# Optimization experiments

Hardware: AMD Instinct MI355X
Metric: run time of the kernel (lower is better)

The kernel has to match this reference:

```python
import jax, jax.numpy as jnp
import numpy as np

V, BLK, C, H, L = 50257, 1024, 1024, 16, 4
B, T = 2, 1024
D = C // H
EPS = 1e-5

def _ln(x, w):
    mu = jnp.mean(x, axis=-1, keepdims=True)
    var = jnp.mean(jnp.square(x - mu), axis=-1, keepdims=True)
    return (x - mu) * jax.lax.rsqrt(var + EPS) * w

def setup_inputs() -> dict:
    key = jax.random.key(0)
    ks = jax.random.split(key, 9)
    s = 0.02
    return {
        'idx': jax.random.randint(ks[0], (B, T), 0, V),
        'wte': jax.random.normal(ks[1], (V, C), jnp.float32) * s,
        'wpe': jax.random.normal(ks[2], (BLK, C), jnp.float32) * s,
        'ln1_w': jnp.ones((L, C), jnp.float32),
        'attn_w': jax.random.normal(ks[3], (L, 3 * C, C), jnp.float32) * s,   # torch Linear [out,in]
        'attnproj_w': jax.random.normal(ks[4], (L, C, C), jnp.float32) * (s / np.sqrt(2 * L)),
        'ln2_w': jnp.ones((L, C), jnp.float32),
        'fc_w': jax.random.normal(ks[5], (L, 4 * C, C), jnp.float32) * s,
        'mlpproj_w': jax.random.normal(ks[6], (L, C, 4 * C), jnp.float32) * (s / np.sqrt(2 * L)),
        'lnf_w': jnp.ones((C,), jnp.float32),
        'head_w': jax.random.normal(ks[7], (V, C), jnp.float32) * s,
    }

def _block(x, ln1_w, attn_w, attnproj_w, ln2_w, fc_w, mlpproj_w):
    b, t, c = x.shape
    h = _ln(x, ln1_w)
    qkv = h @ attn_w.T                                  # [B,T,3C]
    q, k, v = jnp.split(qkv, 3, axis=-1)
    q = q.reshape(b, t, H, D).transpose(0, 2, 1, 3)      # [B,H,T,D]
    k = k.reshape(b, t, H, D).transpose(0, 2, 1, 3)
    v = v.reshape(b, t, H, D).transpose(0, 2, 1, 3)
    att = jnp.einsum('bhqd,bhkd->bhqk', q, k) * (1.0 / np.sqrt(D))
    causal = jnp.tril(jnp.ones((t, t), bool))
    att = jnp.where(causal, att, jnp.float32(-jnp.inf))
    p = jax.nn.softmax(att, axis=-1)
    y = jnp.einsum('bhqk,bhkd->bhqd', p, v)
    y = y.transpose(0, 2, 1, 3).reshape(b, t, c)
    y = y @ attnproj_w.T
    x = x + y
    m = _ln(x, ln2_w)
    m = jax.nn.relu(m @ fc_w.T) @ mlpproj_w.T
    return x + m

def reference(idx, wte, wpe, ln1_w, attn_w, attnproj_w, ln2_w, fc_w, mlpproj_w, lnf_w, head_w):
    t = idx.shape[1]
    x = wte[idx] + wpe[:t]                               # [B,T,C]
    for i in range(L):
        x = _block(x, ln1_w[i], attn_w[i], attnproj_w[i], ln2_w[i], fc_w[i], mlpproj_w[i])
    x = _ln(x, lnf_w)
    return x @ head_w.T                                  # logits [B,T,V]
```

## Files before the change

### kernel.cpp

```cpp
#include <hip/hip_runtime.h>

typedef __bf16 bf16x8 __attribute__((ext_vector_type(8)));
typedef float f32x4 __attribute__((ext_vector_type(4)));
typedef unsigned short u16x8 __attribute__((ext_vector_type(8)));

#define LOG2E 1.4426950408889634f

__device__ __forceinline__ unsigned short f2bf(float f) {
  union { float f; unsigned u; } v; v.f = f;
  return (unsigned short)((v.u + 0x7fffu + ((v.u >> 16) & 1u)) >> 16);
}

__device__ __forceinline__ void gload16(const void* g, void* l) {
  __builtin_amdgcn_global_load_lds(
      (const __attribute__((address_space(1))) unsigned int*)g,
      (__attribute__((address_space(3))) unsigned int*)l, 16, 0, 0);
}

__global__ __launch_bounds__(256) void cvt_kernel(
    const float* __restrict__ s, unsigned short* __restrict__ d, int n8) {
  int i = blockIdx.x * 256 + threadIdx.x;
  int stride = gridDim.x * 256;
  for (; i < n8; i += stride) {
    float4 a = ((const float4*)s)[2 * i];
    float4 b = ((const float4*)s)[2 * i + 1];
    u16x8 o;
    o[0] = f2bf(a.x); o[1] = f2bf(a.y); o[2] = f2bf(a.z); o[3] = f2bf(a.w);
    o[4] = f2bf(b.x); o[5] = f2bf(b.y); o[6] = f2bf(b.z); o[7] = f2bf(b.w);
    ((u16x8*)d)[i] = o;
  }
}

__global__ __launch_bounds__(256) void embed_kernel(
    const int* __restrict__ idx, const float* __restrict__ wte,
    const float* __restrict__ wpe, float* __restrict__ x) {
  int row = blockIdx.x;
  int tok = idx[row];
  int t = row & 1023;
  float4 a = ((const float4*)(wte + (size_t)tok * 1024))[threadIdx.x];
  float4 p = ((const float4*)(wpe + (size_t)t * 1024))[threadIdx.x];
  a.x += p.x; a.y += p.y; a.z += p.z; a.w += p.w;
  ((float4*)(x + (size_t)row * 1024))[threadIdx.x] = a;
}

__global__ __launch_bounds__(256) void ln_kernel(
    const float* __restrict__ x, const float* __restrict__ w,
    unsigned short* __restrict__ out) {
  __shared__ float2 red[4];
  int row = blockIdx.x, tid = threadIdx.x;
  float4 v = ((const float4*)(x + (size_t)row * 1024))[tid];
  float s  = v.x + v.y + v.z + v.w;
  float s2 = v.x * v.x + v.y * v.y + v.z * v.z + v.w * v.w;
#pragma unroll
  for (int m = 32; m >= 1; m >>= 1) {
    s  += __shfl_xor(s, m, 64);
    s2 += __shfl_xor(s2, m, 64);
  }
  if ((tid & 63) == 0) red[tid >> 6] = make_float2(s, s2);
  __syncthreads();
  float S = 0.f, S2 = 0.f;
#pragma unroll
  for (int i = 0; i < 4; ++i) { S += red[i].x; S2 += red[i].y; }
  float mu = S * (1.f / 1024.f);
  float var = S2 * (1.f / 1024.f) - mu * mu;
  float rs = rsqrtf(var + 1e-5f);
  float4 wv = ((const float4*)w)[tid];
  ushort4 o;
  o.x = f2bf((v.x - mu) * rs * wv.x);
  o.y = f2bf((v.y - mu) * rs * wv.y);
  o.z = f2bf((v.z - mu) * rs * wv.z);
  o.w = f2bf((v.w - mu) * rs * wv.w);
  ((ushort4*)(out + (size_t)row * 1024))[tid] = o;
}

template <int MODE, bool WB16>
__global__ __launch_bounds__(256, 2) void gemm_bt(
    const unsigned short* __restrict__ A, const void* __restrict__ Wp,
    void* __restrict__ outp, const float* __restrict__ resid,
    unsigned short* __restrict__ qo, unsigned short* __restrict__ ko,
    unsigned short* __restrict__ vo, int M, int N, int K) {
  __shared__ unsigned short As[2][128 * 64];
  __shared__ unsigned short Bs[2][128 * 64];

  const int tid = threadIdx.x;
  const int lane = tid & 63;
  const int wv = tid >> 6;
  const int lr = lane & 15, lh = lane >> 4;
  const int nbm = M >> 7;
  const int nb = gridDim.x;
  const int bid = blockIdx.x;
  const int swz = (bid & 7) * (nb >> 3) + (bid >> 3);
  const int m0 = (swz % nbm) << 7;
  const int n0 = (swz / nbm) << 7;
  const int wm = (wv >> 1) << 6;
  const int wn = (wv & 1) << 6;
  const int nK = K >> 6;

  float4 breg[8];
  const float* Wf = (const float*)Wp;
  const unsigned short* Wb = (const unsigned short*)Wp;

  auto loadB = [&](int kt) {
#pragma unroll
    for (int j = 0; j < 8; ++j) {
      int u = j * 256 + tid;
      int rn = n0 + (u >> 4);
      if (rn >= N) rn = N - 1;
      breg[j] = *(const float4*)(Wf + (size_t)rn * K + kt * 64 + (u & 15) * 4);
    }
  };
  auto writeB = [&](int buf) {
#pragma unroll
    for (int j = 0; j < 8; ++j) {
      int u = j * 256 + tid;
      int row = u >> 4, q = u & 15;
      ushort4 h4;
      h4.x = f2bf(breg[j].x); h4.y = f2bf(breg[j].y);
      h4.z = f2bf(breg[j].z); h4.w = f2bf(breg[j].w);
      int off = row * 128 + ((q * 8) ^ ((row & 7) << 4));
      *(ushort4*)((char*)(&Bs[buf][0]) + off) = h4;
    }
  };
  auto stageA = [&](int buf, int kt) {
    const unsigned short* base = A + (size_t)m0 * K + kt * 64;
#pragma unroll
    for (int j = 0; j < 4; ++j) {
      int u = j * 256 + tid;
      int row = u >> 3, un = u & 7;
      gload16(base + (size_t)row * K + ((un ^ (row & 7)) << 3),
              (char*)(&As[buf][0]) + u * 16);
    }
  };
  auto stageB16 = [&](int buf, int kt) {
#pragma unroll
    for (int j = 0; j < 4; ++j) {
      int u = j * 256 + tid;
      int row = u >> 3, un = u & 7;
      size_t grow = (size_t)(n0 + row);
      if constexpr (MODE == 4) { if ((int)grow >= N) grow = N - 1; }
      gload16(Wb + grow * K + kt * 64 + ((un ^ (row & 7)) << 3),
              (char*)(&Bs[buf][0]) + u * 16);
    }
  };

  f32x4 acc[4][4];
#pragma unroll
  for (int a = 0; a < 4; ++a)
#pragma unroll
    for (int b = 0; b < 4; ++b) acc[a][b] = f32x4{0.f, 0.f, 0.f, 0.f};

  if constexpr (WB16) {
    stageA(0, 0);
    stageB16(0, 0);
  } else {
    loadB(0);
    stageA(0, 0);
    writeB(0);
  }
  __syncthreads();

  for (int kt = 0; kt < nK; ++kt) {
    int cur = kt & 1;
    if constexpr (WB16) {
      if (kt + 1 < nK) { stageA(cur ^ 1, kt + 1); stageB16(cur ^ 1, kt + 1); }
    } else {
      if (kt + 1 < nK) { loadB(kt + 1); stageA(cur ^ 1, kt + 1); }
    }

    bf16x8 af[4][2], bf[4][2];
#pragma unroll
    for (int mi = 0; mi < 4; ++mi)
#pragma unroll
      for (int ks = 0; ks < 2; ++ks) {
        int row = wm + mi * 16 + lr;
        int off = row * 128 + ((ks * 64 + lh * 16) ^ ((row & 7) << 4));
        af[mi][ks] = *(const bf16x8*)((const char*)(&As[cur][0]) + off);
      }
#pragma unroll
    for (int ni = 0; ni < 4; ++ni)
#pragma unroll
      for (int ks = 0; ks < 2; ++ks) {
        int row = wn + ni * 16 + lr;
        int off = row * 128 + ((ks * 64 + lh * 16) ^ ((row & 7) << 4));
        bf[ni][ks] = *(const bf16x8*)((const char*)(&Bs[cur][0]) + off);
      }
#pragma unroll
    for (int ks = 0; ks < 2; ++ks)
#pragma unroll
      for (int mi = 0; mi < 4; ++mi)
#pragma unroll
        for (int ni = 0; ni < 4; ++ni)
          acc[mi][ni] = __builtin_amdgcn_mfma_f32_16x16x32_bf16(
              af[mi][ks], bf[ni][ks], acc[mi][ni], 0, 0, 0);

    if constexpr (!WB16) {
      if (kt + 1 < nK) writeB(cur ^ 1);
    }
    __syncthreads();
  }

#pragma unroll
  for (int mi = 0; mi < 4; ++mi)
#pragma unroll
    for (int ni = 0; ni < 4; ++ni)
#pragma unroll
      for (int r = 0; r < 4; ++r) {
        int grow = m0 + wm + mi * 16 + lh * 4 + r;
        int gcol = n0 + wn + ni * 16 + lr;
        float val = acc[mi][ni][r];
        if constexpr (MODE == 1) val = fmaxf(val, 0.f);
        if constexpr (MODE == 0 || MODE == 1) {
          ((unsigned short*)outp)[(size_t)grow * N + gcol] = f2bf(val);
        } else if constexpr (MODE == 2) {
          ((float*)outp)[(size_t)grow * N + gcol] =
              resid[(size_t)grow * N + gcol] + val;
        } else if constexpr (MODE == 3) {
          int which = gcol >> 10, hh = (gcol >> 6) & 15, dd = gcol & 63;
          int b = grow >> 10, t = grow & 1023;
          unsigned short hv = f2bf(val);
          size_t bh = (size_t)(b * 16 + hh) << 16;
          if (which == 0)      qo[bh + t * 64 + dd] = hv;
          else if (which == 1) ko[bh + t * 64 + dd] = hv;
          else                 vo[bh + dd * 1024 + t] = hv;
        } else {
          if (gcol < N)
            ((float*)outp)[(size_t)grow * (size_t)N + gcol] = val;
        }
      }
}

template <int MODE>
__global__ __launch_bounds__(256, 2) void gemm128_bt(
    const unsigned short* __restrict__ A, const unsigned short* __restrict__ Wb,
    void* __restrict__ outp, const float* __restrict__ resid,
    unsigned short* __restrict__ qo, unsigned short* __restrict__ ko,
    unsigned short* __restrict__ vo, int M, int N, int K) {
  __shared__ unsigned short As[4][128 * 32];
  __shared__ unsigned short Bs[4][128 * 32];

  const int tid = threadIdx.x;
  const int lane = tid & 63;
  const int wv = tid >> 6;
  const int lr = lane & 15, lh = lane >> 4;
  const int nbm = M >> 7;
  const int nb = gridDim.x;
  const int bid = blockIdx.x;
  const int swz = (bid & 7) * (nb >> 3) + (bid >> 3);
  const int m0 = (swz % nbm) << 7;
  const int n0 = (swz / nbm) << 7;
  const int wm = (wv >> 1) << 6;
  const int wn = (wv & 1) << 6;
  const int nK = K >> 5;

  size_t aoff[2], boff[2];
  int ldst[2];
#pragma unroll
  for (int j = 0; j < 2; ++j) {
    int u = j * 256 + tid;
    int p = u >> 3, s = u & 7;
    int ss = s ^ (p & 7);
    int arow = m0 + 2 * p + (ss >> 2);
    int brow = n0 + 2 * p + (ss >> 2);
    if (brow >= N) brow = N - 1;
    aoff[j] = (size_t)arow * K + (ss & 3) * 8;
    boff[j] = (size_t)brow * K + (ss & 3) * 8;
    ldst[j] = u * 16;
  }

  auto stage = [&](int buf, int k) {
#pragma unroll
    for (int j = 0; j < 2; ++j)
      gload16(A + aoff[j] + k * 32, (char*)(&As[buf][0]) + ldst[j]);
#pragma unroll
    for (int j = 0; j < 2; ++j)
      gload16(Wb + boff[j] + k * 32, (char*)(&Bs[buf][0]) + ldst[j]);
  };

  f32x4 acc[4][4];
#pragma unroll
  for (int a = 0; a < 4; ++a)
#pragma unroll
    for (int b = 0; b < 4; ++b) acc[a][b] = f32x4{0.f, 0.f, 0.f, 0.f};

  stage(0, 0);
  if (nK > 1) stage(1, 1);
  if (nK > 2) stage(2, 2);
  if (nK > 2)      asm volatile("s_waitcnt vmcnt(8)" ::: "memory");
  else if (nK > 1) asm volatile("s_waitcnt vmcnt(4)" ::: "memory");
  else             asm volatile("s_waitcnt vmcnt(0)" ::: "memory");
  __builtin_amdgcn_s_barrier();
  __builtin_amdgcn_sched_barrier(0);

  for (int kt = 0; kt < nK; ++kt) {
    const int buf = kt & 3;
    bf16x8 af[4], bfr[4];
#pragma unroll
    for (int ni = 0; ni < 4; ++ni) {
      int r = wn + ni * 16 + lr;
      int p = r >> 1;
      int off = p * 128 + (((((r & 1) << 2) | lh) ^ (p & 7)) << 4);
      bfr[ni] = *(const bf16x8*)((const char*)(&Bs[buf][0]) + off);
    }
#pragma unroll
    for (int mi = 0; mi < 4; ++mi) {
      int r = wm + mi * 16 + lr;
      int p = r >> 1;
      int off = p * 128 + (((((r & 1) << 2) | lh) ^ (p & 7)) << 4);
      af[mi] = *(const bf16x8*)((const char*)(&As[buf][0]) + off);
    }
    if (kt + 3 < nK) stage((kt + 3) & 3, kt + 3);

    __builtin_amdgcn_s_setprio(1);
#pragma unroll
    for (int mi = 0; mi < 4; ++mi)
#pragma unroll
      for (int ni = 0; ni < 4; ++ni)
        acc[mi][ni] = __builtin_amdgcn_mfma_f32_16x16x32_bf16(
            af[mi], bfr[ni], acc[mi][ni], 0, 0, 0);
    __builtin_amdgcn_s_setprio(0);

    if (kt + 1 < nK) {
      if (kt + 4 <= nK)      asm volatile("s_waitcnt vmcnt(8)" ::: "memory");
      else if (kt + 3 <= nK) asm volatile("s_waitcnt vmcnt(4)" ::: "memory");
      else                   asm volatile("s_waitcnt vmcnt(0)" ::: "memory");
      __builtin_amdgcn_s_barrier();
      __builtin_amdgcn_sched_barrier(0);
    }
  }

#pragma unroll
  for (int mi = 0; mi < 4; ++mi)
#pragma unroll
    for (int ni = 0; ni < 4; ++ni)
#pragma unroll
      for (int r = 0; r < 4; ++r) {
        int grow = m0 + wm + mi * 16 + lh * 4 + r;
        int gcol = n0 + wn + ni * 16 + lr;
        float val = acc[mi][ni][r];
        if constexpr (MODE == 1) val = fmaxf(val, 0.f);
        if constexpr (MODE == 0 || MODE == 1) {
          ((unsigned short*)outp)[(size_t)grow * N + gcol] = f2bf(val);
        } else if constexpr (MODE == 2) {
          ((float*)outp)[(size_t)grow * N + gcol] =
              resid[(size_t)grow * N + gcol] + val;
        } else if constexpr (MODE == 3) {
          int which = gcol >> 10, hh = (gcol >> 6) & 15, dd = gcol & 63;
          int b = grow >> 10, t = grow & 1023;
          unsigned short hv = f2bf(val);
          size_t bh = (size_t)(b * 16 + hh) << 16;
          if (which == 0)      qo[bh + t * 64 + dd] = hv;
          else if (which == 1) ko[bh + t * 64 + dd] = hv;
          else                 vo[bh + dd * 1024 + t] = hv;
        } else {
          if (gcol < N)
            ((float*)outp)[(size_t)grow * (size_t)N + gcol] = val;
        }
      }
}

template <int MODE>
__global__ __launch_bounds__(256, 2) void gemm64n_bt(
    const unsigned short* __restrict__ A, const unsigned short* __restrict__ Wb,
    void* __restrict__ outp, const float* __restrict__ resid,
    unsigned short* __restrict__ qo, unsigned short* __restrict__ ko,
    unsigned short* __restrict__ vo, int M, int N, int K) {
  __shared__ unsigned short As[4][128 * 32];
  __shared__ unsigned short Bs[4][64 * 32];

  const int tid = threadIdx.x;
  const int lane = tid & 63;
  const int wv = tid >> 6;
  const int lr = lane & 15, lh = lane >> 4;
  const int nbm = M >> 7;
  const int nb = gridDim.x;
  const int bid = blockIdx.x;
  const int swz = (bid & 7) * (nb >> 3) + (bid >> 3);
  const int m0 = (swz % nbm) << 7;
  const int n0 = (swz / nbm) << 6;
  const int wm = (wv >> 1) << 6;
  const int wn = (wv & 1) << 5;
  const int nK = K >> 5;

  size_t aoff[2], boff;
  int ldsta[2], ldstb;
#pragma unroll
  for (int j = 0; j < 2; ++j) {
    int u = j * 256 + tid;
    int p = u >> 3, s = u & 7;
    int ss = s ^ (p & 7);
    int arow = m0 + 2 * p + (ss >> 2);
    aoff[j] = (size_t)arow * K + (ss & 3) * 8;
    ldsta[j] = u * 16;
  }
  {
    int u = tid;
    int p = u >> 3, s = u & 7;
    int ss = s ^ (p & 7);
    int brow = n0 + 2 * p + (ss >> 2);
    if (brow >= N) brow = N - 1;
    boff = (size_t)brow * K + (ss & 3) * 8;
    ldstb = u * 16;
  }

  auto stage = [&](int buf, int k) {
#pragma unroll
    for (int j = 0; j < 2; ++j)
      gload16(A + aoff[j] + k * 32, (char*)(&As[buf][0]) + ldsta[j]);
    gload16(Wb + boff + k * 32, (char*)(&Bs[buf][0]) + ldstb);
  };

  f32x4 acc[4][2];
#pragma unroll
  for (int a = 0; a < 4; ++a)
#pragma unroll
    for (int b = 0; b < 2; ++b) acc[a][b] = f32x4{0.f, 0.f, 0.f, 0.f};

  stage(0, 0);
  if (nK > 1) stage(1, 1);
  if (nK > 2) stage(2, 2);
  if (nK > 2)      asm volatile("s_waitcnt vmcnt(6)" ::: "memory");
  else if (nK > 1) asm volatile("s_waitcnt vmcnt(3)" ::: "memory");
  else             asm volatile("s_waitcnt vmcnt(0)" ::: "memory");
  __builtin_amdgcn_s_barrier();
  __builtin_amdgcn_sched_barrier(0);

  for (int kt = 0; kt < nK; ++kt) {
    const int buf = kt & 3;
    bf16x8 af[4], bfr[2];
#pragma unroll
    for (int ni = 0; ni < 2; ++ni) {
      int r = wn + ni * 16 + lr;
      int p = r >> 1;
      int off = p * 128 + (((((r & 1) << 2) | lh) ^ (p & 7)) << 4);
      bfr[ni] = *(const bf16x8*)((const char*)(&Bs[buf][0]) + off);
    }
#pragma unroll
    for (int mi = 0; mi < 4; ++mi) {
      int r = wm + mi * 16 + lr;
      int p = r >> 1;
      int off = p * 128 + (((((r & 1) << 2) | lh) ^ (p & 7)) << 4);
      af[mi] = *(const bf16x8*)((const char*)(&As[buf][0]) + off);
    }
    if (kt + 3 < nK) stage((kt + 3) & 3, kt + 3);

    __builtin_amdgcn_s_setprio(1);
#pragma unroll
    for (int mi = 0; mi < 4; ++mi)
#pragma unroll
      for (int ni = 0; ni < 2; ++ni)
        acc[mi][ni] = __builtin_amdgcn_mfma_f32_16x16x32_bf16(
            af[mi], bfr[ni], acc[mi][ni], 0, 0, 0);
    __builtin_amdgcn_s_setprio(0);

    if (kt + 1 < nK) {
      if (kt + 4 <= nK)      asm volatile("s_waitcnt vmcnt(6)" ::: "memory");
      else if (kt + 3 <= nK) asm volatile("s_waitcnt vmcnt(3)" ::: "memory");
      else                   asm volatile("s_waitcnt vmcnt(0)" ::: "memory");
      __builtin_amdgcn_s_barrier();
      __builtin_amdgcn_sched_barrier(0);
    }
  }

#pragma unroll
  for (int mi = 0; mi < 4; ++mi)
#pragma unroll
    for (int ni = 0; ni < 2; ++ni)
#pragma unroll
      for (int r = 0; r < 4; ++r) {
        int grow = m0 + wm + mi * 16 + lh * 4 + r;
        int gcol = n0 + wn + ni * 16 + lr;
        float val = acc[mi][ni][r];
        if constexpr (MODE == 1) val = fmaxf(val, 0.f);
        if constexpr (MODE == 0 || MODE == 1) {
          ((unsigned short*)outp)[(size_t)grow * N + gcol] = f2bf(val);
        } else if constexpr (MODE == 2) {
          ((float*)outp)[(size_t)grow * N + gcol] =
              resid[(size_t)grow * N + gcol] + val;
        } else if constexpr (MODE == 3) {
          int which = gcol >> 10, hh = (gcol >> 6) & 15, dd = gcol & 63;
          int b = grow >> 10, t = grow & 1023;
          unsigned short hv = f2bf(val);
          size_t bh = (size_t)(b * 16 + hh) << 16;
          if (which == 0)      qo[bh + t * 64 + dd] = hv;
          else if (which == 1) ko[bh + t * 64 + dd] = hv;
          else                 vo[bh + dd * 1024 + t] = hv;
        } else {
          if (gcol < N)
            ((float*)outp)[(size_t)grow * (size_t)N + gcol] = val;
        }
      }
}

__global__ __launch_bounds__(512, 2) void gemm256_bt(
    const unsigned short* __restrict__ A, const unsigned short* __restrict__ Wb,
    float* __restrict__ out, int M, int N, int K) {
  __shared__ unsigned short As[4][256 * 32];
  __shared__ unsigned short Bs[4][256 * 32];

  const int tid = threadIdx.x;
  const int lane = tid & 63;
  const int wv = tid >> 6;
  const int lr = lane & 15, lh = lane >> 4;
  const int wm = (wv >> 2) * 128;
  const int wn = (wv & 3) * 64;
  const int nbm = M >> 8;
  const int nb = gridDim.x;
  const int bid = blockIdx.x;
  const int swz = (bid & 7) * (nb >> 3) + (bid >> 3);
  const int m0 = (swz % nbm) << 8;
  const int n0 = (swz / nbm) << 8;
  const int nK = K >> 5;

  size_t aoff[2], boff[2];
  int ldst[2];
#pragma unroll
  for (int j = 0; j < 2; ++j) {
    int u = j * 512 + tid;
    int p = u >> 3, s = u & 7;
    int ss = s ^ (p & 7);
    int arow = m0 + 2 * p + (ss >> 2);
    int brow = n0 + 2 * p + (ss >> 2);
    if (brow >= N) brow = N - 1;
    aoff[j] = (size_t)arow * K + (ss & 3) * 8;
    boff[j] = (size_t)brow * K + (ss & 3) * 8;
    ldst[j] = u * 16;
  }

  auto stage = [&](int buf, int k) {
#pragma unroll
    for (int j = 0; j < 2; ++j)
      gload16(A + aoff[j] + k * 32, (char*)(&As[buf][0]) + ldst[j]);
#pragma unroll
    for (int j = 0; j < 2; ++j)
      gload16(Wb + boff[j] + k * 32, (char*)(&Bs[buf][0]) + ldst[j]);
  };

  f32x4 acc[8][4];
#pragma unroll
  for (int a = 0; a < 8; ++a)
#pragma unroll
    for (int b = 0; b < 4; ++b) acc[a][b] = f32x4{0.f, 0.f, 0.f, 0.f};

  stage(0, 0);
  if (nK > 1) stage(1, 1);
  if (nK > 2) stage(2, 2);
  if (nK > 2) asm volatile("s_waitcnt vmcnt(8)" ::: "memory");
  else        asm volatile("s_waitcnt vmcnt(0)" ::: "memory");
  __builtin_amdgcn_s_barrier();
  __builtin_amdgcn_sched_barrier(0);

  for (int k = 0; k < nK; ++k) {
    const int buf = k & 3;
    bf16x8 af[8], bfr[4];
#pragma unroll
    for (int ni = 0; ni < 4; ++ni) {
      int r = wn + ni * 16 + lr;
      int p = r >> 1;
      int off = p * 128 + (((((r & 1) << 2) | lh) ^ (p & 7)) << 4);
      bfr[ni] = *(const bf16x8*)((const char*)(&Bs[buf][0]) + off);
    }
#pragma unroll
    for (int mi = 0; mi < 8; ++mi) {
      int r = wm + mi * 16 + lr;
      int p = r >> 1;
      int off = p * 128 + (((((r & 1) << 2) | lh) ^ (p & 7)) << 4);
      af[mi] = *(const bf16x8*)((const char*)(&As[buf][0]) + off);
    }
    if (k + 3 < nK) stage((k + 3) & 3, k + 3);

    __builtin_amdgcn_s_setprio(1);
#pragma unroll
    for (int mi = 0; mi < 8; ++mi)
#pragma unroll
      for (int ni = 0; ni < 4; ++ni)
        acc[mi][ni] = __builtin_amdgcn_mfma_f32_16x16x32_bf16(
            af[mi], bfr[ni], acc[mi][ni], 0, 0, 0);
    __builtin_amdgcn_s_setprio(0);

    if (k + 1 < nK) {
      if (k + 4 <= nK)      asm volatile("s_waitcnt vmcnt(8)" ::: "memory");
      else if (k + 3 <= nK) asm volatile("s_waitcnt vmcnt(4)" ::: "memory");
      else                  asm volatile("s_waitcnt vmcnt(0)" ::: "memory");
      __builtin_amdgcn_s_barrier();
      __builtin_amdgcn_sched_barrier(0);
    }
  }

#pragma unroll
  for (int mi = 0; mi < 8; ++mi)
#pragma unroll
    for (int ni = 0; ni < 4; ++ni)
#pragma unroll
      for (int r = 0; r < 4; ++r) {
        int grow = m0 + wm + mi * 16 + lh * 4 + r;
        int gcol = n0 + wn + ni * 16 + lr;
        if (gcol < N) out[(size_t)grow * (size_t)N + gcol] = acc[mi][ni][r];
      }
}

__global__ __launch_bounds__(128, 2) void attn_kernel(
    const unsigned short* __restrict__ qb, const unsigned short* __restrict__ kb,
    const unsigned short* __restrict__ vt, unsigned short* __restrict__ yb) {
  __shared__ unsigned short Ks[2][64 * 64];
  __shared__ unsigned short Vs[2][64 * 64];
  __shared__ unsigned short Ps[2][32 * 64];

  const int tid = threadIdx.x, lane = tid & 63, wv = tid >> 6;
  const int lr = lane & 15, lh = lane >> 4;
  const int bid = blockIdx.x;
  const int bh = bid & 31;
  const int rest = bid >> 5;
  const int j = rest >> 1, hf = rest & 1;
  const int sub = (hf * 2 + wv) * 16;
  const int rb0 = j * 64 + sub;
  const int rb1 = (15 - j) * 64 + sub;
  const unsigned short* qp = qb + ((size_t)bh << 16);
  const unsigned short* kp = kb + ((size_t)bh << 16);
  const unsigned short* vp = vt + ((size_t)bh << 16);

  bf16x8 qf[2][2];
#pragma unroll
  for (int mi = 0; mi < 2; ++mi)
#pragma unroll
    for (int ks = 0; ks < 2; ++ks) {
      int row = (mi ? rb1 : rb0) + lr;
      qf[mi][ks] = *(const bf16x8*)(qp + (size_t)row * 64 + ks * 32 + lh * 8);
    }

  f32x4 o[2][4];
  float mr[2][4], lsum[2][4];
#pragma unroll
  for (int mi = 0; mi < 2; ++mi) {
#pragma unroll
    for (int di = 0; di < 4; ++di) o[mi][di] = f32x4{0.f, 0.f, 0.f, 0.f};
#pragma unroll
    for (int r = 0; r < 4; ++r) { mr[mi][r] = -1e30f; lsum[mi][r] = 0.f; }
  }

  const int ntiles = 16 - j;

  auto stageKV = [&](int buf, int t) {
    int kv0 = t << 6;
#pragma unroll
    for (int jj = 0; jj < 4; ++jj) {
      int u = jj * 128 + tid;
      int row = u >> 3, un = u & 7;
      gload16(kp + (size_t)(kv0 + row) * 64 + ((un ^ (row & 7)) << 3),
              (char*)(&Ks[buf][0]) + u * 16);
      gload16(vp + (size_t)row * 1024 + kv0 + ((un ^ (row & 7)) << 3),
              (char*)(&Vs[buf][0]) + u * 16);
    }
  };

  stageKV(0, 0);

  for (int t = 0; t < ntiles; ++t) {
    __syncthreads();
    if (t + 1 < ntiles) stageKV((t + 1) & 1, t + 1);
    int cur = t & 1;
    int kv0 = t << 6;
    const bool act0 = (t <= j);

    f32x4 s[2][4];
#pragma unroll
    for (int mi = 0; mi < 2; ++mi)
#pragma unroll
      for (int ni = 0; ni < 4; ++ni) s[mi][ni] = f32x4{0.f, 0.f, 0.f, 0.f};

    bf16x8 kf[4][2];
#pragma unroll
    for (int ni = 0; ni < 4; ++ni)
#pragma unroll
      for (int ks = 0; ks < 2; ++ks) {
        int row = ni * 16 + lr;
        int off = row * 128 + ((ks * 64 + lh * 16) ^ ((row & 7) << 4));
        kf[ni][ks] = *(const bf16x8*)((const char*)(&Ks[cur][0]) + off);
      }
#pragma unroll
    for (int ks = 0; ks < 2; ++ks)
#pragma unroll
      for (int ni = 0; ni < 4; ++ni) {
        if (act0)
          s[0][ni] = __builtin_amdgcn_mfma_f32_16x16x32_bf16(
              qf[0][ks], kf[ni][ks], s[0][ni], 0, 0, 0);
        s[1][ni] = __builtin_amdgcn_mfma_f32_16x16x32_bf16(
            qf[1][ks], kf[ni][ks], s[1][ni], 0, 0, 0);
      }

#pragma unroll
    for (int mi = 0; mi < 2; ++mi) {
      if (mi == 0 && !act0) continue;
      const int rb = mi ? rb1 : rb0;
#pragma unroll
      for (int r = 0; r < 4; ++r) {
        int rowq = rb + lh * 4 + r;
        float xv[4];
        float pm = -1e30f;
#pragma unroll
        for (int ni = 0; ni < 4; ++ni) {
          int col = kv0 + ni * 16 + lr;
          float xx = s[mi][ni][r] * 0.125f;
          if (col > rowq) xx = -1e30f;
          xv[ni] = xx;
          pm = fmaxf(pm, xx);
        }
#pragma unroll
        for (int msk = 1; msk < 16; msk <<= 1)
          pm = fmaxf(pm, __shfl_xor(pm, msk, 64));
        float mnew = fmaxf(mr[mi][r], pm);
        float al = exp2f((mr[mi][r] - mnew) * LOG2E);
        mr[mi][r] = mnew;
        float ps = 0.f;
#pragma unroll
        for (int ni = 0; ni < 4; ++ni) {
          float p = exp2f((xv[ni] - mnew) * LOG2E);
          s[mi][ni][r] = p;
          ps += p;
        }
#pragma unroll
        for (int msk = 1; msk < 16; msk <<= 1) ps += __shfl_xor(ps, msk, 64);
        lsum[mi][r] = lsum[mi][r] * al + ps;
#pragma unroll
        for (int di = 0; di < 4; ++di) o[mi][di][r] *= al;
      }
    }

#pragma unroll
    for (int mi = 0; mi < 2; ++mi) {
      if (mi == 0 && !act0) continue;
#pragma unroll
      for (int ni = 0; ni < 4; ++ni)
#pragma unroll
        for (int r = 0; r < 4; ++r) {
          int row = mi * 16 + lh * 4 + r;
          int off = row * 128 + (((ni * 16 + lr) * 2) ^ ((row & 7) << 4));
          *(unsigned short*)((char*)(&Ps[wv][0]) + off) = f2bf(s[mi][ni][r]);
        }
    }

    bf16x8 pf[2][2], vf[4][2];
#pragma unroll
    for (int mi = 0; mi < 2; ++mi) {
      if (mi == 0 && !act0) continue;
#pragma unroll
      for (int ks = 0; ks < 2; ++ks) {
        int row = mi * 16 + lr;
        int off = row * 128 + ((ks * 64 + lh * 16) ^ ((row & 7) << 4));
        pf[mi][ks] = *(const bf16x8*)((const char*)(&Ps[wv][0]) + off);
      }
    }
#pragma unroll
    for (int di = 0; di < 4; ++di)
#pragma unroll
      for (int ks = 0; ks < 2; ++ks) {
        int row = di * 16 + lr;
        int off = row * 128 + ((ks * 64 + lh * 16) ^ ((row & 7) << 4));
        vf[di][ks] = *(const bf16x8*)((const char*)(&Vs[cur][0]) + off);
      }
#pragma unroll
    for (int ks = 0; ks < 2; ++ks)
#pragma unroll
      for (int di = 0; di < 4; ++di) {
        if (act0)
          o[0][di] = __builtin_amdgcn_mfma_f32_16x16x32_bf16(
              pf[0][ks], vf[di][ks], o[0][di], 0, 0, 0);
        o[1][di] = __builtin_amdgcn_mfma_f32_16x16x32_bf16(
            pf[1][ks], vf[di][ks], o[1][di], 0, 0, 0);
      }
  }

  int b = bh >> 4, hh = bh & 15;
#pragma unroll
  for (int mi = 0; mi < 2; ++mi)
#pragma unroll
    for (int r = 0; r < 4; ++r) {
      float inv = 1.f / lsum[mi][r];
      int rowq = (mi ? rb1 : rb0) + lh * 4 + r;
      size_t mg = (size_t)(b * 1024 + rowq) * 1024 + hh * 64;
#pragma unroll
      for (int di = 0; di < 4; ++di)
        yb[mg + di * 16 + lr] = f2bf(o[mi][di][r] * inv);
    }
}

extern "C" void kernel_launch(void* const* d_in, const int* in_sizes, int n_in,
                              void* d_out, int out_size, void* d_ws,
                              size_t ws_size, hipStream_t stream) {
  const int*   idx  = (const int*)d_in[0];
  const float* wte  = (const float*)d_in[1];
  const float* wpe  = (const float*)d_in[2];
  const float* ln1w = (const float*)d_in[3];
  const float* attnw= (const float*)d_in[4];
  const float* aprj = (const float*)d_in[5];
  const float* ln2w = (const float*)d_in[6];
  const float* fcw  = (const float*)d_in[7];
  const float* mprj = (const float*)d_in[8];
  const float* lnfw = (const float*)d_in[9];
  const float* hw   = (const float*)d_in[10];
  float* out = (float*)d_out;
  char* ws = (char*)d_ws;

  float* x            = (float*)ws;
  unsigned short* h   = (unsigned short*)(ws + ((size_t)8 << 20));
  unsigned short* qbf = (unsigned short*)(ws + ((size_t)12 << 20));
  unsigned short* kbf = (unsigned short*)(ws + ((size_t)16 << 20));
  unsigned short* vtb = (unsigned short*)(ws + ((size_t)20 << 20));
  unsigned short* ybf = (unsigned short*)(ws + ((size_t)24 << 20));
  unsigned short* mhb = (unsigned short*)(ws + ((size_t)12 << 20));

  size_t off = (size_t)28 << 20;
  unsigned short* attnw16 = (unsigned short*)(ws + off); off += (size_t)4 * 3072 * 1024 * 2;
  unsigned short* aprj16  = (unsigned short*)(ws + off); off += (size_t)4 * 1024 * 1024 * 2;
  unsigned short* fcw16   = (unsigned short*)(ws + off); off += (size_t)4 * 4096 * 1024 * 2;
  unsigned short* mprj16  = (unsigned short*)(ws + off); off += (size_t)4 * 1024 * 4096 * 2;
  unsigned short* hw16    = (unsigned short*)(ws + off); off += (size_t)50257 * 1024 * 2;
  const bool b16 = ws_size >= off;

  embed_kernel<<<2048, 256, 0, stream>>>(idx, wte, wpe, x);

  if (b16) {
    cvt_kernel<<<2048, 256, 0, stream>>>(attnw, attnw16, 4 * 3072 * 1024 / 8);
    cvt_kernel<<<2048, 256, 0, stream>>>(aprj,  aprj16,  4 * 1024 * 1024 / 8);
    cvt_kernel<<<2048, 256, 0, stream>>>(fcw,   fcw16,   4 * 4096 * 1024 / 8);
    cvt_kernel<<<2048, 256, 0, stream>>>(mprj,  mprj16,  4 * 1024 * 4096 / 8);
    cvt_kernel<<<2048, 256, 0, stream>>>(hw,    hw16,    50257 * 1024 / 8);
  }

  for (int l = 0; l < 4; ++l) {
    ln_kernel<<<2048, 256, 0, stream>>>(x, ln1w + l * 1024, h);
    if (b16)
      gemm64n_bt<3><<<16 * 48, 256, 0, stream>>>(
          h, attnw16 + (size_t)l * 3072 * 1024, nullptr, nullptr, qbf, kbf,
          vtb, 2048, 3072, 1024);
    else
      gemm_bt<3, false><<<16 * 24, 256, 0, stream>>>(
          h, attnw + (size_t)l * 3072 * 1024, nullptr, nullptr, qbf, kbf, vtb,
          2048, 3072, 1024);
    attn_kernel<<<512, 128, 0, stream>>>(qbf, kbf, vtb, ybf);
    if (b16)
      gemm64n_bt<2><<<16 * 16, 256, 0, stream>>>(
          ybf, aprj16 + (size_t)l * 1024 * 1024, x, x, nullptr, nullptr,
          nullptr, 2048, 1024, 1024);
    else
      gemm_bt<2, false><<<16 * 8, 256, 0, stream>>>(
          ybf, aprj + (size_t)l * 1024 * 1024, x, x, nullptr, nullptr, nullptr,
          2048, 1024, 1024);
    ln_kernel<<<2048, 256, 0, stream>>>(x, ln2w + l * 1024, h);
    if (b16)
      gemm128_bt<1><<<16 * 32, 256, 0, stream>>>(
          h, fcw16 + (size_t)l * 4096 * 1024, mhb, nullptr, nullptr, nullptr,
          nullptr, 2048, 4096, 1024);
    else
      gemm_bt<1, false><<<16 * 32, 256, 0, stream>>>(
          h, fcw + (size_t)l * 4096 * 1024, mhb, nullptr, nullptr, nullptr,
          nullptr, 2048, 4096, 1024);
    if (b16)
      gemm64n_bt<2><<<16 * 16, 256, 0, stream>>>(
          mhb, mprj16 + (size_t)l * 1024 * 4096, x, x, nullptr, nullptr,
          nullptr, 2048, 1024, 4096);
    else
      gemm_bt<2, false><<<16 * 8, 256, 0, stream>>>(
          mhb, mprj + (size_t)l * 1024 * 4096, x, x, nullptr, nullptr, nullptr,
          2048, 1024, 4096);
  }

  ln_kernel<<<2048, 256, 0, stream>>>(x, lnfw, h);
  if (b16)
    gemm256_bt<<<8 * 197, 512, 0, stream>>>(h, hw16, out, 2048, 50257, 1024);
  else
    gemm_bt<4, false><<<16 * 393, 256, 0, stream>>>(
        h, hw, out, nullptr, nullptr, nullptr, nullptr, 2048, 50257, 1024);
}
```

Measured before the change: 1.202 ms.

## Merge weight conversion launches and shrink head GEMM to double buffering

Replaces the five separate fp32-to-bf16 weight conversion launches with one kernel that walks all five segments in turn, removing launch overhead and tail gaps between them. Separately, the 256x256 head GEMM goes from a 4-stage LDS pipeline with three tiles in flight to a 2-stage double buffer that prefetches only the next tile and waits on all loads each step. This halves LDS use per block, which may help occupancy. The cost is much less memory-latency hiding in the large head GEMM.

Result: slower. 1.273 ms (+5.9%).

```diff
diff --git a/kernel.cpp b/kernel.cpp
--- a/kernel.cpp
+++ b/kernel.cpp
@@ -17,17 +17,29 @@
       (__attribute__((address_space(3))) unsigned int*)l, 16, 0, 0);
 }
 
-__global__ __launch_bounds__(256) void cvt_kernel(
-    const float* __restrict__ s, unsigned short* __restrict__ d, int n8) {
-  int i = blockIdx.x * 256 + threadIdx.x;
+__global__ __launch_bounds__(256) void cvt5_kernel(
+    const float* __restrict__ s0, unsigned short* __restrict__ d0, int n0,
+    const float* __restrict__ s1, unsigned short* __restrict__ d1, int n1,
+    const float* __restrict__ s2, unsigned short* __restrict__ d2, int n2,
+    const float* __restrict__ s3, unsigned short* __restrict__ d3, int n3,
+    const float* __restrict__ s4, unsigned short* __restrict__ d4, int n4) {
   int stride = gridDim.x * 256;
-  for (; i < n8; i += stride) {
-    float4 a = ((const float4*)s)[2 * i];
-    float4 b = ((const float4*)s)[2 * i + 1];
-    u16x8 o;
-    o[0] = f2bf(a.x); o[1] = f2bf(a.y); o[2] = f2bf(a.z); o[3] = f2bf(a.w);
-    o[4] = f2bf(b.x); o[5] = f2bf(b.y); o[6] = f2bf(b.z); o[7] = f2bf(b.w);
-    ((u16x8*)d)[i] = o;
+  const float* ss[5] = {s0, s1, s2, s3, s4};
+  unsigned short* dd[5] = {d0, d1, d2, d3, d4};
+  int nn[5] = {n0, n1, n2, n3, n4};
+#pragma unroll
+  for (int seg = 0; seg < 5; ++seg) {
+    const float* s = ss[seg];
+    unsigned short* d = dd[seg];
+    int n8 = nn[seg];
+    for (int i = blockIdx.x * 256 + threadIdx.x; i < n8; i += stride) {
+      float4 a = ((const float4*)s)[2 * i];
+      float4 b = ((const float4*)s)[2 * i + 1];
+      u16x8 o;
+      o[0] = f2bf(a.x); o[1] = f2bf(a.y); o[2] = f2bf(a.z); o[3] = f2bf(a.w);
+      o[4] = f2bf(b.x); o[5] = f2bf(b.y); o[6] = f2bf(b.z); o[7] = f2bf(b.w);
+      ((u16x8*)d)[i] = o;
+    }
   }
 }
 
@@ -494,8 +506,8 @@
 __global__ __launch_bounds__(512, 2) void gemm256_bt(
     const unsigned short* __restrict__ A, const unsigned short* __restrict__ Wb,
     float* __restrict__ out, int M, int N, int K) {
-  __shared__ unsigned short As[4][256 * 32];
-  __shared__ unsigned short Bs[4][256 * 32];
+  __shared__ unsigned short As[2][256 * 32];
+  __shared__ unsigned short Bs[2][256 * 32];
 
   const int tid = threadIdx.x;
   const int lane = tid & 63;
@@ -542,15 +554,14 @@
     for (int b = 0; b < 4; ++b) acc[a][b] = f32x4{0.f, 0.f, 0.f, 0.f};
 
   stage(0, 0);
-  if (nK > 1) stage(1, 1);
-  if (nK > 2) stage(2, 2);
-  if (nK > 2) asm volatile("s_waitcnt vmcnt(8)" ::: "memory");
-  else        asm volatile("s_waitcnt vmcnt(0)" ::: "memory");
+  asm volatile("s_waitcnt vmcnt(0)" ::: "memory");
   __builtin_amdgcn_s_barrier();
   __builtin_amdgcn_sched_barrier(0);
 
   for (int k = 0; k < nK; ++k) {
-    const int buf = k & 3;
+    const int buf = k & 1;
+    if (k + 1 < nK) stage(buf ^ 1, k + 1);
+
     bf16x8 af[8], bfr[4];
 #pragma unroll
     for (int ni = 0; ni < 4; ++ni) {
@@ -566,7 +577,6 @@
       int off = p * 128 + (((((r & 1) << 2) | lh) ^ (p & 7)) << 4);
       af[mi] = *(const bf16x8*)((const char*)(&As[buf][0]) + off);
     }
-    if (k + 3 < nK) stage((k + 3) & 3, k + 3);
 
     __builtin_amdgcn_s_setprio(1);
 #pragma unroll
@@ -578,9 +588,7 @@
     __builtin_amdgcn_s_setprio(0);
 
     if (k + 1 < nK) {
-      if (k + 4 <= nK)      asm volatile("s_waitcnt vmcnt(8)" ::: "memory");
-      else if (k + 3 <= nK) asm volatile("s_waitcnt vmcnt(4)" ::: "memory");
-      else                  asm volatile("s_waitcnt vmcnt(0)" ::: "memory");
+      asm volatile("s_waitcnt vmcnt(0)" ::: "memory");
       __builtin_amdgcn_s_barrier();
       __builtin_amdgcn_sched_barrier(0);
     }
@@ -819,11 +827,12 @@
   embed_kernel<<<2048, 256, 0, stream>>>(idx, wte, wpe, x);
 
   if (b16) {
-    cvt_kernel<<<2048, 256, 0, stream>>>(attnw, attnw16, 4 * 3072 * 1024 / 8);
-    cvt_kernel<<<2048, 256, 0, stream>>>(aprj,  aprj16,  4 * 1024 * 1024 / 8);
-    cvt_kernel<<<2048, 256, 0, stream>>>(fcw,   fcw16,   4 * 4096 * 1024 / 8);
-    cvt_kernel<<<2048, 256, 0, stream>>>(mprj,  mprj16,  4 * 1024 * 4096 / 8);
-    cvt_kernel<<<2048, 256, 0, stream>>>(hw,    hw16,    50257 * 1024 / 8);
+    cvt5_kernel<<<2048, 256, 0, stream>>>(
+        attnw, attnw16, 4 * 3072 * 1024 / 8,
+        aprj,  aprj16,  4 * 1024 * 1024 / 8,
+        fcw,   fcw16,   4 * 4096 * 1024 / 8,
+        mprj,  mprj16,  4 * 1024 * 4096 / 8,
+        hw,    hw16,    50257 * 1024 / 8);
   }
 
   for (int l = 0; l < 4; ++l) {
```
